# Kernel optimization log

Measured on AMD Instinct MI355X. Metric: run time of the kernel, lower is better.

## Reference

```python
import jax, jax.numpy as jnp
import numpy as np

B = 131072
D = 64
NUM_REL = 32


def setup_inputs() -> dict:
    key = jax.random.key(0)
    k1, k2, k3, k4 = jax.random.split(key, 4)
    embeds1 = jax.random.normal(k1, (B, D), dtype=jnp.float32)
    embeds2 = jax.random.normal(k2, (B, D), dtype=jnp.float32)
    rels = jax.random.randint(k3, (B,), 0, NUM_REL, dtype=jnp.int32)
    # learned relation table: one D*D matrix per relation type
    rel_embeds = jax.random.normal(k4, (NUM_REL, D * D), dtype=jnp.float32)
    return {"embeds1": embeds1, "embeds2": embeds2, "rels": rels,
            "rel_embeds": rel_embeds}


def reference(embeds1, embeds2, rels, rel_embeds):
    # gather per-sample relation matrices: [B, D, D]
    rel_mats = rel_embeds[rels].reshape(-1, D, D)
    # per-sample bilinear form: score_b = e1_b^T R_b e2_b  -> [B]
    e1R = jnp.einsum("bd,bde->be", embeds1, rel_mats)
    return (e1R * embeds2).sum(axis=1)
```

## Files before the change

### kernel.cpp

```cpp
#include <hip/hip_runtime.h>
#include <hip/hip_bf16.h>
#include <cstddef>

#define BB 131072
#define DD 64
#define NREL 32

#define CAP 4608
#define TILES (CAP / 64)
#define BLKX (TILES / 4)
#define PERM_SLOTS (NREL * CAP)

#define SCB 256
#define SCT 512
#define CSTRIDE 16

#define RSTR 72

typedef __attribute__((ext_vector_type(8))) __bf16 bf16x8;
typedef __attribute__((ext_vector_type(16))) float f32x16;

__global__ __launch_bounds__(SCT) void scatter_atomic(
    const int* __restrict__ rels, int* __restrict__ cursor,
    int* __restrict__ perm) {
  __shared__ int hist[NREL];
  __shared__ int base[NREL];
  const int t = threadIdx.x;
  if (t < NREL) hist[t] = 0;
  __syncthreads();
  const int s = blockIdx.x * SCT + t;
  const int rv = rels[s];
  const int rank = atomicAdd(&hist[rv], 1);
  __syncthreads();
  if (t < NREL) base[t] = atomicAdd(&cursor[t * CSTRIDE], hist[t]);
  __syncthreads();
  perm[rv * CAP + base[rv] + rank] = s;
}

__global__ __launch_bounds__(256, 4) void bilinear_mfma(
    const float* __restrict__ e1g, const float* __restrict__ e2g,
    const float* __restrict__ relE, const int* __restrict__ perm,
    const int* __restrict__ cursor, float* __restrict__ out) {
  __shared__ float smem[4 * 64 * 33];
  __bf16* RH = (__bf16*)smem;
  __bf16* RL = RH + 64 * RSTR;
  const int t = threadIdx.x;
  const int r0 = blockIdx.y;
  const int end = cursor[r0 * CSTRIDE];
  const int tile0 = blockIdx.x * 4;
  if (tile0 * 64 >= end) return;

  const int wid = t >> 6;
  const int lane = t & 63;
  const int h = lane >> 5;
  const int l31 = lane & 31;
  const int slot = (tile0 + wid) * 64 + lane;
  const bool valid = slot < end;
  const int pk = perm[r0 * CAP + slot] & 0x1FFFF;
  const int rowid0 = __shfl(pk, l31);
  const int rowid1 = __shfl(pk, 32 + l31);

  {
    const float* Rg = relE + (size_t)r0 * (DD * DD);
    const int k = t >> 2;
    const int n0 = (t & 3) * 16;
    float4 x[4];
#pragma unroll
    for (int i = 0; i < 4; ++i)
      x[i] = *(const float4*)(Rg + (size_t)k * DD + n0 + 4 * i);
    const float* xs = (const float*)x;
#pragma unroll
    for (int j = 0; j < 16; ++j) {
      const float v = xs[j];
      const __bf16 hb = (__bf16)v;
      RH[(n0 + j) * RSTR + k] = hb;
      RL[(n0 + j) * RSTR + k] = (__bf16)(v - (float)hb);
    }
  }
  __syncthreads();

  f32x16 acc[2][2];
#pragma unroll
  for (int ti = 0; ti < 2; ++ti)
#pragma unroll
    for (int tj = 0; tj < 2; ++tj)
#pragma unroll
      for (int i = 0; i < 16; ++i) acc[ti][tj][i] = 0.f;

#pragma unroll
  for (int kc = 0; kc < 4; ++kc) {
    bf16x8 aH[2], aL[2], bH[2], bL[2];
#pragma unroll
    for (int ti = 0; ti < 2; ++ti) {
      const float* ap =
          e1g + (size_t)(ti ? rowid1 : rowid0) * DD + kc * 16 + 8 * h;
      const float4 x0 = *(const float4*)(ap);
      const float4 x1 = *(const float4*)(ap + 4);
      const float xs[8] = {x0.x, x0.y, x0.z, x0.w, x1.x, x1.y, x1.z, x1.w};
#pragma unroll
      for (int j = 0; j < 8; ++j) {
        const __bf16 hb = (__bf16)xs[j];
        aH[ti][j] = hb;
        aL[ti][j] = (__bf16)(xs[j] - (float)hb);
      }
    }
#pragma unroll
    for (int tj = 0; tj < 2; ++tj) {
      const int bo = (32 * tj + l31) * RSTR + kc * 16 + 8 * h;
      bH[tj] = *(const bf16x8*)(RH + bo);
      bL[tj] = *(const bf16x8*)(RL + bo);
    }
#pragma unroll
    for (int ti = 0; ti < 2; ++ti)
#pragma unroll
      for (int tj = 0; tj < 2; ++tj) {
        acc[ti][tj] = __builtin_amdgcn_mfma_f32_32x32x16_bf16(aH[ti], bH[tj], acc[ti][tj], 0, 0, 0);
        acc[ti][tj] = __builtin_amdgcn_mfma_f32_32x32x16_bf16(aH[ti], bL[tj], acc[ti][tj], 0, 0, 0);
        acc[ti][tj] = __builtin_amdgcn_mfma_f32_32x32x16_bf16(aL[ti], bH[tj], acc[ti][tj], 0, 0, 0);
      }
  }

  __syncthreads();

  float* sP = smem + wid * (64 * 33);
#pragma unroll
  for (int ti = 0; ti < 2; ++ti)
#pragma unroll
    for (int g = 0; g < 4; ++g)
#pragma unroll
      for (int q = 0; q < 4; ++q) {
        const int reg = g * 4 + q;
        const int rbase = 32 * ti + q + 8 * g;
        const int s0 = __builtin_amdgcn_readlane(pk, rbase);
        const int s1 = __builtin_amdgcn_readlane(pk, rbase + 4);
        const int bs = h ? s1 : s0;
        const float* er = e2g + (size_t)bs * DD + l31;
        const float v = fmaf(acc[ti][0][reg], er[0], acc[ti][1][reg] * er[32]);
        sP[(rbase + 4 * h) * 33 + l31] = v;
      }
  __syncthreads();
  float sc = 0.f;
#pragma unroll
  for (int c = 0; c < 32; ++c) sc += sP[lane * 33 + c];
  if (valid) out[pk] = sc;
}

extern "C" void kernel_launch(void* const* d_in, const int* in_sizes, int n_in,
                              void* d_out, int out_size, void* d_ws, size_t ws_size,
                              hipStream_t stream) {
  const float* e1 = (const float*)d_in[0];
  const float* e2 = (const float*)d_in[1];
  const int* rels = (const int*)d_in[2];
  const float* relE = (const float*)d_in[3];
  float* out = (float*)d_out;

  int* perm = (int*)d_ws;
  int* cursor = perm + PERM_SLOTS;

  hipMemsetAsync(cursor, 0, NREL * CSTRIDE * sizeof(int), stream);
  scatter_atomic<<<SCB, SCT, 0, stream>>>(rels, cursor, perm);
  bilinear_mfma<<<dim3(BLKX, NREL), 256, 0, stream>>>(e1, e2, relE, perm,
                                                      cursor, out);
}
```

Measured before the change: 113.5 us.

## Prefetch all e1 rows before relation staging and use 3-wave blocks

```diff
diff --git a/kernel.cpp b/kernel.cpp
--- a/kernel.cpp
+++ b/kernel.cpp
@@ -8,7 +8,9 @@
 
 #define CAP 4608
 #define TILES (CAP / 64)
-#define BLKX (TILES / 4)
+#define BWAVES 3
+#define TPB (BWAVES * 64)
+#define BLKX (TILES / BWAVES)
 #define PERM_SLOTS (NREL * CAP)
 
 #define SCB 256
@@ -37,17 +39,17 @@
   perm[rv * CAP + base[rv] + rank] = s;
 }
 
-__global__ __launch_bounds__(256, 4) void bilinear_mfma(
+__global__ __launch_bounds__(TPB, 3) void bilinear_mfma(
     const float* __restrict__ e1g, const float* __restrict__ e2g,
     const float* __restrict__ relE, const int* __restrict__ perm,
     const int* __restrict__ cursor, float* __restrict__ out) {
-  __shared__ float smem[4 * 64 * 33];
+  __shared__ float smem[BWAVES * 64 * 33];
   __bf16* RH = (__bf16*)smem;
   __bf16* RL = RH + 64 * RSTR;
   const int t = threadIdx.x;
   const int r0 = blockIdx.y;
   const int end = cursor[r0 * CSTRIDE];
-  const int tile0 = blockIdx.x * 4;
+  const int tile0 = blockIdx.x * BWAVES;
   if (tile0 * 64 >= end) return;
 
   const int wid = t >> 6;
@@ -60,21 +62,41 @@
   const int rowid0 = __shfl(pk, l31);
   const int rowid1 = __shfl(pk, 32 + l31);
 
+  bf16x8 aH[2][4], aL[2][4];
+#pragma unroll
+  for (int ti = 0; ti < 2; ++ti) {
+    const float* rowp = e1g + (size_t)(ti ? rowid1 : rowid0) * DD + 8 * h;
+#pragma unroll
+    for (int kc = 0; kc < 4; ++kc) {
+      const float* ap = rowp + kc * 16;
+      const float4 x0 = *(const float4*)(ap);
+      const float4 x1 = *(const float4*)(ap + 4);
+      const float xs[8] = {x0.x, x0.y, x0.z, x0.w, x1.x, x1.y, x1.z, x1.w};
+#pragma unroll
+      for (int j = 0; j < 8; ++j) {
+        const __bf16 hb = (__bf16)xs[j];
+        aH[ti][kc][j] = hb;
+        aL[ti][kc][j] = (__bf16)(xs[j] - (float)hb);
+      }
+    }
+  }
+
   {
     const float* Rg = relE + (size_t)r0 * (DD * DD);
-    const int k = t >> 2;
     const int n0 = (t & 3) * 16;
-    float4 x[4];
+    for (int kk = (t >> 2); kk < 64; kk += 48) {
+      float4 x[4];
 #pragma unroll
-    for (int i = 0; i < 4; ++i)
-      x[i] = *(const float4*)(Rg + (size_t)k * DD + n0 + 4 * i);
-    const float* xs = (const float*)x;
+      for (int i = 0; i < 4; ++i)
+        x[i] = *(const float4*)(Rg + (size_t)kk * DD + n0 + 4 * i);
+      const float* xs = (const float*)x;
 #pragma unroll
-    for (int j = 0; j < 16; ++j) {
-      const float v = xs[j];
-      const __bf16 hb = (__bf16)v;
-      RH[(n0 + j) * RSTR + k] = hb;
-      RL[(n0 + j) * RSTR + k] = (__bf16)(v - (float)hb);
+      for (int j = 0; j < 16; ++j) {
+        const float v = xs[j];
+        const __bf16 hb = (__bf16)v;
+        RH[(n0 + j) * RSTR + kk] = hb;
+        RL[(n0 + j) * RSTR + kk] = (__bf16)(v - (float)hb);
+      }
     }
   }
   __syncthreads();
@@ -89,21 +111,7 @@
 
 #pragma unroll
   for (int kc = 0; kc < 4; ++kc) {
-    bf16x8 aH[2], aL[2], bH[2], bL[2];
-#pragma unroll
-    for (int ti = 0; ti < 2; ++ti) {
-      const float* ap =
-          e1g + (size_t)(ti ? rowid1 : rowid0) * DD + kc * 16 + 8 * h;
-      const float4 x0 = *(const float4*)(ap);
-      const float4 x1 = *(const float4*)(ap + 4);
-      const float xs[8] = {x0.x, x0.y, x0.z, x0.w, x1.x, x1.y, x1.z, x1.w};
-#pragma unroll
-      for (int j = 0; j < 8; ++j) {
-        const __bf16 hb = (__bf16)xs[j];
-        aH[ti][j] = hb;
-        aL[ti][j] = (__bf16)(xs[j] - (float)hb);
-      }
-    }
+    bf16x8 bH[2], bL[2];
 #pragma unroll
     for (int tj = 0; tj < 2; ++tj) {
       const int bo = (32 * tj + l31) * RSTR + kc * 16 + 8 * h;
@@ -114,9 +122,9 @@
     for (int ti = 0; ti < 2; ++ti)
 #pragma unroll
       for (int tj = 0; tj < 2; ++tj) {
-        acc[ti][tj] = __builtin_amdgcn_mfma_f32_32x32x16_bf16(aH[ti], bH[tj], acc[ti][tj], 0, 0, 0);
-        acc[ti][tj] = __builtin_amdgcn_mfma_f32_32x32x16_bf16(aH[ti], bL[tj], acc[ti][tj], 0, 0, 0);
-        acc[ti][tj] = __builtin_amdgcn_mfma_f32_32x32x16_bf16(aL[ti], bH[tj], acc[ti][tj], 0, 0, 0);
+        acc[ti][tj] = __builtin_amdgcn_mfma_f32_32x32x16_bf16(aH[ti][kc], bH[tj], acc[ti][tj], 0, 0, 0);
+        acc[ti][tj] = __builtin_amdgcn_mfma_f32_32x32x16_bf16(aH[ti][kc], bL[tj], acc[ti][tj], 0, 0, 0);
+        acc[ti][tj] = __builtin_amdgcn_mfma_f32_32x32x16_bf16(aL[ti][kc], bH[tj], acc[ti][tj], 0, 0, 0);
       }
   }
 
@@ -159,6 +167,6 @@
 
   hipMemsetAsync(cursor, 0, NREL * CSTRIDE * sizeof(int), stream);
   scatter_atomic<<<SCB, SCT, 0, stream>>>(rels, cursor, perm);
-  bilinear_mfma<<<dim3(BLKX, NREL), 256, 0, stream>>>(e1, e2, relE, perm,
+  bilinear_mfma<<<dim3(BLKX, NREL), TPB, 0, stream>>>(e1, e2, relE, perm,
                                                       cursor, out);
 }
```

Result: faster. 106.8 us (-6.0%).

## Shrink per-wave tile to 32 samples and prefetch e1 rows before R staging

Applied to the files above, without the earlier changes.

```diff
diff --git a/kernel.cpp b/kernel.cpp
--- a/kernel.cpp
+++ b/kernel.cpp
@@ -7,8 +7,9 @@
 #define NREL 32
 
 #define CAP 4608
-#define TILES (CAP / 64)
-#define BLKX (TILES / 4)
+#define SPW 32
+#define SPB 128
+#define BLKX (CAP / SPB)
 #define PERM_SLOTS (NREL * CAP)
 
 #define SCB 256
@@ -41,24 +42,34 @@
     const float* __restrict__ e1g, const float* __restrict__ e2g,
     const float* __restrict__ relE, const int* __restrict__ perm,
     const int* __restrict__ cursor, float* __restrict__ out) {
-  __shared__ float smem[4 * 64 * 33];
+  __shared__ float smem[4608];
   __bf16* RH = (__bf16*)smem;
   __bf16* RL = RH + 64 * RSTR;
   const int t = threadIdx.x;
   const int r0 = blockIdx.y;
   const int end = cursor[r0 * CSTRIDE];
-  const int tile0 = blockIdx.x * 4;
-  if (tile0 * 64 >= end) return;
+  const int sbBlk = blockIdx.x * SPB;
+  if (sbBlk >= end) return;
 
   const int wid = t >> 6;
   const int lane = t & 63;
   const int h = lane >> 5;
   const int l31 = lane & 31;
-  const int slot = (tile0 + wid) * 64 + lane;
-  const bool valid = slot < end;
+  const int slot = sbBlk + wid * SPW + l31;
+  const bool valid = (slot < end) & (h == 0);
   const int pk = perm[r0 * CAP + slot] & 0x1FFFF;
-  const int rowid0 = __shfl(pk, l31);
-  const int rowid1 = __shfl(pk, 32 + l31);
+
+  float a[4][8];
+  {
+    const float* rowp = e1g + (size_t)pk * DD + 8 * h;
+#pragma unroll
+    for (int kc = 0; kc < 4; ++kc) {
+      const float4 x0 = *(const float4*)(rowp + kc * 16);
+      const float4 x1 = *(const float4*)(rowp + kc * 16 + 4);
+      a[kc][0] = x0.x; a[kc][1] = x0.y; a[kc][2] = x0.z; a[kc][3] = x0.w;
+      a[kc][4] = x1.x; a[kc][5] = x1.y; a[kc][6] = x1.z; a[kc][7] = x1.w;
+    }
+  }
 
   {
     const float* Rg = relE + (size_t)r0 * (DD * DD);
@@ -79,69 +90,53 @@
   }
   __syncthreads();
 
-  f32x16 acc[2][2];
+  f32x16 acc[2];
 #pragma unroll
-  for (int ti = 0; ti < 2; ++ti)
+  for (int tj = 0; tj < 2; ++tj)
 #pragma unroll
-    for (int tj = 0; tj < 2; ++tj)
-#pragma unroll
-      for (int i = 0; i < 16; ++i) acc[ti][tj][i] = 0.f;
+    for (int i = 0; i < 16; ++i) acc[tj][i] = 0.f;
 
 #pragma unroll
   for (int kc = 0; kc < 4; ++kc) {
-    bf16x8 aH[2], aL[2], bH[2], bL[2];
+    bf16x8 aH, aL;
 #pragma unroll
-    for (int ti = 0; ti < 2; ++ti) {
-      const float* ap =
-          e1g + (size_t)(ti ? rowid1 : rowid0) * DD + kc * 16 + 8 * h;
-      const float4 x0 = *(const float4*)(ap);
-      const float4 x1 = *(const float4*)(ap + 4);
-      const float xs[8] = {x0.x, x0.y, x0.z, x0.w, x1.x, x1.y, x1.z, x1.w};
-#pragma unroll
-      for (int j = 0; j < 8; ++j) {
-        const __bf16 hb = (__bf16)xs[j];
-        aH[ti][j] = hb;
-        aL[ti][j] = (__bf16)(xs[j] - (float)hb);
-      }
+    for (int j = 0; j < 8; ++j) {
+      const __bf16 hb = (__bf16)a[kc][j];
+      aH[j] = hb;
+      aL[j] = (__bf16)(a[kc][j] - (float)hb);
     }
 #pragma unroll
     for (int tj = 0; tj < 2; ++tj) {
       const int bo = (32 * tj + l31) * RSTR + kc * 16 + 8 * h;
-      bH[tj] = *(const bf16x8*)(RH + bo);
-      bL[tj] = *(const bf16x8*)(RL + bo);
+      const bf16x8 bH = *(const bf16x8*)(RH + bo);
+      const bf16x8 bL = *(const bf16x8*)(RL + bo);
+      acc[tj] = __builtin_amdgcn_mfma_f32_32x32x16_bf16(aH, bH, acc[tj], 0, 0, 0);
+      acc[tj] = __builtin_amdgcn_mfma_f32_32x32x16_bf16(aH, bL, acc[tj], 0, 0, 0);
+      acc[tj] = __builtin_amdgcn_mfma_f32_32x32x16_bf16(aL, bH, acc[tj], 0, 0, 0);
     }
-#pragma unroll
-    for (int ti = 0; ti < 2; ++ti)
-#pragma unroll
-      for (int tj = 0; tj < 2; ++tj) {
-        acc[ti][tj] = __builtin_amdgcn_mfma_f32_32x32x16_bf16(aH[ti], bH[tj], acc[ti][tj], 0, 0, 0);
-        acc[ti][tj] = __builtin_amdgcn_mfma_f32_32x32x16_bf16(aH[ti], bL[tj], acc[ti][tj], 0, 0, 0);
-        acc[ti][tj] = __builtin_amdgcn_mfma_f32_32x32x16_bf16(aL[ti], bH[tj], acc[ti][tj], 0, 0, 0);
-      }
   }
 
   __syncthreads();
 
-  float* sP = smem + wid * (64 * 33);
+  float* sP = smem + wid * (SPW * 33);
 #pragma unroll
-  for (int ti = 0; ti < 2; ++ti)
+  for (int g = 0; g < 4; ++g)
 #pragma unroll
-    for (int g = 0; g < 4; ++g)
-#pragma unroll
-      for (int q = 0; q < 4; ++q) {
-        const int reg = g * 4 + q;
-        const int rbase = 32 * ti + q + 8 * g;
-        const int s0 = __builtin_amdgcn_readlane(pk, rbase);
-        const int s1 = __builtin_amdgcn_readlane(pk, rbase + 4);
-        const int bs = h ? s1 : s0;
-        const float* er = e2g + (size_t)bs * DD + l31;
-        const float v = fmaf(acc[ti][0][reg], er[0], acc[ti][1][reg] * er[32]);
-        sP[(rbase + 4 * h) * 33 + l31] = v;
-      }
+    for (int q = 0; q < 4; ++q) {
+      const int reg = g * 4 + q;
+      const int rbase = q + 8 * g;
+      const int s0 = __builtin_amdgcn_readlane(pk, rbase);
+      const int s1 = __builtin_amdgcn_readlane(pk, rbase + 4);
+      const int bs = h ? s1 : s0;
+      const float* er = e2g + (size_t)bs * DD + l31;
+      const float v = fmaf(acc[0][reg], er[0], acc[1][reg] * er[32]);
+      sP[(rbase + 4 * h) * 33 + l31] = v;
+    }
   __syncthreads();
   float sc = 0.f;
 #pragma unroll
-  for (int c = 0; c < 32; ++c) sc += sP[lane * 33 + c];
+  for (int c = 0; c < 16; ++c) sc += sP[l31 * 33 + 16 * h + c];
+  sc += __shfl_xor(sc, 32);
   if (valid) out[pk] = sc;
 }
 
```

Result: faster. 108.6 us (-4.4%).
